# Optimization experiments

Measured on AMD Instinct MI355X. Metric: run time of the kernel, lower is better.

## Reference

```python
import jax, jax.numpy as jnp
import numpy as np

MARGIN = 0.2
LAMBDA_CLS = 1.0
LAMBDA_TRIPLET = 1.0
EPS = 1e-6  # matches torch pairwise_distance eps inside TripletMarginLoss
B, D, C = 8192, 192, 1024


def setup_inputs() -> dict:
    key = jax.random.key(0)
    k1, k2, k3 = jax.random.split(key, 3)
    embeddings = jax.random.normal(k1, (B, D), dtype=jnp.float32)
    logits = jax.random.normal(k2, (B, C), dtype=jnp.float32)
    targets = jax.random.randint(k3, (B,), 0, C, dtype=jnp.int64)
    return {"embeddings": embeddings, "logits": logits, "targets": targets}


def reference(embeddings, logits, targets):
    # ---- classification loss: mean cross entropy ----
    logp = jax.nn.log_softmax(logits, axis=-1)
    cls_loss = -jnp.mean(jnp.take_along_axis(logp, targets[:, None], axis=1))

    # ---- vectorized hard triplet mining (mining='hard'), on detached embeddings ----
    e = jax.lax.stop_gradient(embeddings)
    sq = jnp.sum(e * e, axis=1)                       # [B]
    d2 = sq[:, None] + sq[None, :] - 2.0 * (e @ e.T)  # [B, B]
    dist = jnp.sqrt(jnp.maximum(d2, 0.0))

    same = targets[:, None] == targets[None, :]       # [B, B]
    eye = jnp.eye(targets.shape[0], dtype=bool)
    pos_mask = same & ~eye
    neg_mask = ~same
    valid = pos_mask.any(axis=1) & neg_mask.any(axis=1)

    # hard positive: farthest same-speaker; hard negative: closest other-speaker
    pos_idx = jnp.argmax(jnp.where(pos_mask, dist, -jnp.inf), axis=1)
    neg_idx = jnp.argmin(jnp.where(neg_mask, dist, jnp.inf), axis=1)

    # ---- triplet margin loss on live embeddings ----
    a = embeddings
    p = embeddings[pos_idx]
    n = embeddings[neg_idx]
    d_ap = jnp.linalg.norm(a - p + EPS, axis=1)
    d_an = jnp.linalg.norm(a - n + EPS, axis=1)
    per_triplet = jnp.maximum(d_ap - d_an + MARGIN, 0.0)

    w = valid.astype(per_triplet.dtype)
    cnt = jnp.sum(w)
    trip_loss = jnp.where(cnt > 0, jnp.sum(per_triplet * w) / jnp.maximum(cnt, 1.0), 0.0)

    return LAMBDA_CLS * cls_loss + LAMBDA_TRIPLET * trip_loss
```

## Files before the change

kernel.cpp:

```cpp
#include <hip/hip_runtime.h>
#include <math.h>

#define B_N    8192
#define D_DIM  192
#define C_CLS  1024
#define MARGIN 0.2f
#define EPS_T  1e-6f

#define TI     64
#define TJ     128
#define JSPLIT 16
#define JLEN   (B_N / JSPLIT)
#define RB     384

typedef short v8s  __attribute__((ext_vector_type(8)));
typedef float v16f __attribute__((ext_vector_type(16)));

typedef __attribute__((address_space(3))) unsigned int       lds_u32;
typedef __attribute__((address_space(1))) const unsigned int glb_u32;

__device__ __forceinline__ void gll16(const void* g, void* l) {
  __builtin_amdgcn_global_load_lds((glb_u32*)g, (lds_u32*)l, 16, 0, 0);
}

__device__ __forceinline__ int swzb(int r, int cb) {
  return r * RB + (cb ^ ((r & 7) << 4));
}

__device__ __forceinline__ unsigned fkey(float f) {
  unsigned u = __float_as_uint(f);
  return (u & 0x80000000u) ? ~u : (u | 0x80000000u);
}

__device__ __forceinline__ unsigned short to_bf(float x) {
  unsigned u = __float_as_uint(x);
  u += 0x7fffu + ((u >> 16) & 1u);
  return (unsigned short)(u >> 16);
}

__global__ __launch_bounds__(256) void prep_kernel(
    const float* __restrict__ e, unsigned short* __restrict__ ebf,
    float* __restrict__ sq,
    unsigned long long* __restrict__ posw, unsigned long long* __restrict__ negw,
    float* __restrict__ accum) {
  int w = threadIdx.x >> 6, lane = threadIdx.x & 63;
  int row = blockIdx.x * 4 + w;
  const float* p = e + (size_t)row * D_DIM;
  float v0 = p[lane], v1 = p[lane + 64], v2 = p[lane + 128];
  unsigned short* q = ebf + (size_t)row * D_DIM;
  q[lane] = to_bf(v0); q[lane + 64] = to_bf(v1); q[lane + 128] = to_bf(v2);
  float s = v0 * v0 + v1 * v1 + v2 * v2;
  #pragma unroll
  for (int off = 32; off; off >>= 1) s += __shfl_xor(s, off);
  if (lane == 0) sq[row] = s;
  int b = blockIdx.x;
  if (b < 32)       posw[b * 256 + threadIdx.x] = 0ULL;
  else if (b < 64)  negw[(b - 32) * 256 + threadIdx.x] = ~0ULL;
  else if (b == 64 && threadIdx.x < 4) ((unsigned*)accum)[threadIdx.x] = 0u;
}

__global__ __launch_bounds__(256, 2) void mine_kernel(
    const unsigned short* __restrict__ ebf, const int* __restrict__ tgt,
    const float* __restrict__ sq, const float* __restrict__ logits,
    unsigned long long* __restrict__ posw, unsigned long long* __restrict__ negw,
    float* __restrict__ accum) {
  __shared__ unsigned short lds_b[TJ * (RB / 2)];
  __shared__ int   lds_t[TJ];
  __shared__ float lds_s[TJ];
  __shared__ unsigned long long pmrg[TI];
  __shared__ unsigned long long nmrg[TI];
  __shared__ float ce_part[4];

  const int tid  = threadIdx.x;
  const int w    = tid >> 6;
  const int lane = tid & 63;
  const int n5   = lane & 31;
  const int h    = lane >> 5;
  const int i0 = blockIdx.x * TI;
  const int jb = blockIdx.y * JLEN;

  char* ldsc = (char*)lds_b;

  if (tid < TI) { pmrg[tid] = 0ULL; nmrg[tid] = ~0ULL; }

  {
    const char* src = (const char*)(ebf + (size_t)i0 * D_DIM);
    #pragma unroll
    for (int t = 0; t < 6; ++t) {
      int c  = t * 256 + tid;
      int r  = c / 24;
      int cb = (c - r * 24) * 16;
      gll16(src + r * RB + (cb ^ ((r & 7) << 4)),
            ldsc + (t * 256 + (tid & ~63)) * 16);
    }
  }
  __syncthreads();
  v8s bfrag[2][12];
  #pragma unroll
  for (int tb = 0; tb < 2; ++tb)
    #pragma unroll
    for (int kc = 0; kc < 12; ++kc)
      bfrag[tb][kc] = *(const v8s*)(ldsc + swzb(tb * 32 + n5, kc * 32 + h * 16));

  int my_t[2];
  #pragma unroll
  for (int tb = 0; tb < 2; ++tb) my_t[tb] = tgt[i0 + tb * 32 + n5];

  float    pv[2] = {-3.4e38f, -3.4e38f}, nv[2] = {3.4e38f, 3.4e38f};
  unsigned pi_[2] = {0u, 0u}, ni_[2] = {0xFFFFFFFFu, 0xFFFFFFFFu};

  for (int j0 = jb; j0 < jb + JLEN; j0 += TJ) {
    __syncthreads();
    {
      const char* src = (const char*)(ebf + (size_t)j0 * D_DIM);
      #pragma unroll
      for (int t = 0; t < 12; ++t) {
        int c  = t * 256 + tid;
        int r  = c / 24;
        int cb = (c - r * 24) * 16;
        gll16(src + r * RB + (cb ^ ((r & 7) << 4)),
              ldsc + (t * 256 + (tid & ~63)) * 16);
      }
    }
    if (tid < TJ) { lds_t[tid] = tgt[j0 + tid]; lds_s[tid] = sq[j0 + tid]; }
    __syncthreads();

    v16f acc[2];
    #pragma unroll
    for (int tb = 0; tb < 2; ++tb)
      #pragma unroll
      for (int r = 0; r < 16; ++r) acc[tb][r] = 0.f;

    #pragma unroll
    for (int kc = 0; kc < 12; ++kc) {
      v8s afr = *(const v8s*)(ldsc + swzb(w * 32 + n5, kc * 32 + h * 16));
      acc[0] = __builtin_amdgcn_mfma_f32_32x32x16_bf16(afr, bfrag[0][kc], acc[0], 0, 0, 0);
      acc[1] = __builtin_amdgcn_mfma_f32_32x32x16_bf16(afr, bfrag[1][kc], acc[1], 0, 0, 0);
    }

    #pragma unroll
    for (int p = 0; p < 4; ++p) {
      int jb4 = w * 32 + p * 8 + h * 4;
      float4 s4 = *(const float4*)&lds_s[jb4];
      int4   t4 = *(const int4*)&lds_t[jb4];
      #pragma unroll
      for (int q = 0; q < 4; ++q) {
        float sv = (q == 0) ? s4.x : (q == 1) ? s4.y : (q == 2) ? s4.z : s4.w;
        int   tv = (q == 0) ? t4.x : (q == 1) ? t4.y : (q == 2) ? t4.z : t4.w;
        unsigned jg = (unsigned)(j0 + jb4 + q);
        #pragma unroll
        for (int tb = 0; tb < 2; ++tb) {
          float val = fmaf(acc[tb][p * 4 + q], -2.0f, sv);
          bool same = (tv == my_t[tb]);
          float vp = same ? val : -3.4e38f;
          float vn = same ? 3.4e38f : val;
          if (vp > pv[tb]) { pv[tb] = vp; pi_[tb] = jg; }
          if (vn < nv[tb]) { nv[tb] = vn; ni_[tb] = jg; }
        }
      }
    }
  }

  #pragma unroll
  for (int tb = 0; tb < 2; ++tb) {
    unsigned long long pk =
        ((unsigned long long)fkey(pv[tb]) << 32) | (unsigned long long)(unsigned)(~pi_[tb]);
    unsigned long long nk =
        ((unsigned long long)fkey(nv[tb]) << 32) | (unsigned long long)ni_[tb];
    unsigned long long po = __shfl_xor(pk, 32);
    unsigned long long no = __shfl_xor(nk, 32);
    pk = pk > po ? pk : po;
    nk = nk < no ? nk : no;
    if (h == 0) {
      atomicMax(&pmrg[tb * 32 + n5], pk);
      atomicMin(&nmrg[tb * 32 + n5], nk);
    }
  }
  __syncthreads();
  if (tid < TI) {
    atomicMax(&posw[i0 + tid], pmrg[tid]);
    atomicMin(&negw[i0 + tid], nmrg[tid]);
  }

  {
    int row = (blockIdx.y * 128 + blockIdx.x) * 4 + w;
    const float* lp = logits + (size_t)row * C_CLS;
    float4 x[4];
    #pragma unroll
    for (int t = 0; t < 4; ++t) x[t] = *(const float4*)(lp + lane * 4 + 256 * t);
    float m = -3.4e38f;
    #pragma unroll
    for (int t = 0; t < 4; ++t)
      m = fmaxf(m, fmaxf(fmaxf(x[t].x, x[t].y), fmaxf(x[t].z, x[t].w)));
    #pragma unroll
    for (int off = 32; off; off >>= 1) m = fmaxf(m, __shfl_xor(m, off));
    float s = 0.f;
    #pragma unroll
    for (int t = 0; t < 4; ++t)
      s += __expf(x[t].x - m) + __expf(x[t].y - m) +
           __expf(x[t].z - m) + __expf(x[t].w - m);
    #pragma unroll
    for (int off = 32; off; off >>= 1) s += __shfl_xor(s, off);
    if (lane == 0) ce_part[w] = m + __logf(s) - lp[tgt[row]];
  }
  __syncthreads();
  if (tid == 0)
    atomicAdd(&accum[0], ce_part[0] + ce_part[1] + ce_part[2] + ce_part[3]);
}

__global__ __launch_bounds__(1024) void trip_fin_kernel(
    const float* __restrict__ e,
    const unsigned long long* __restrict__ posw,
    const unsigned long long* __restrict__ negw,
    float* __restrict__ accum, float* __restrict__ out) {
  __shared__ float ssum[16];
  __shared__ float scnt[16];
  int w = threadIdx.x >> 6, lane = threadIdx.x & 63;
  int i = blockIdx.x * 16 + w;
  unsigned long long pp = posw[i], np = negw[i];
  unsigned pidx = ~(unsigned)pp;
  unsigned nidx = (unsigned)np;
  float res = 0.f, c = 0.f;
  if (pp != 0ULL && np != ~0ULL && pidx != (unsigned)i) {
    const float* pa = e + (size_t)i * D_DIM;
    const float* pb = e + (size_t)pidx * D_DIM;
    const float* pc = e + (size_t)nidx * D_DIM;
    float dap = 0.f, dan = 0.f;
    #pragma unroll
    for (int t = 0; t < 3; ++t) {
      int k = lane + 64 * t;
      float av = pa[k];
      float d1 = av - pb[k] + EPS_T;
      float d2 = av - pc[k] + EPS_T;
      dap += d1 * d1;
      dan += d2 * d2;
    }
    #pragma unroll
    for (int off = 32; off; off >>= 1) {
      dap += __shfl_xor(dap, off);
      dan += __shfl_xor(dan, off);
    }
    res = fmaxf(sqrtf(dap) - sqrtf(dan) + MARGIN, 0.f);
    c = 1.f;
  }
  if (lane == 0) { ssum[w] = res; scnt[w] = c; }
  __syncthreads();
  if (threadIdx.x == 0) {
    float a = 0.f, b = 0.f;
    #pragma unroll
    for (int k = 0; k < 16; ++k) { a += ssum[k]; b += scnt[k]; }
    atomicAdd(&accum[1], a);
    atomicAdd(&accum[2], b);
    __threadfence();
    unsigned old = atomicAdd((unsigned*)&accum[3], 1u);
    if (old == 511u) {
      __threadfence();
      float cls = atomicAdd(&accum[0], 0.f);
      float ts  = atomicAdd(&accum[1], 0.f);
      float tc  = atomicAdd(&accum[2], 0.f);
      float trip = (tc > 0.f) ? ts / fmaxf(tc, 1.f) : 0.f;
      out[0] = cls / (float)B_N + trip;
    }
  }
}

extern "C" void kernel_launch(void* const* d_in, const int* in_sizes, int n_in,
                              void* d_out, int out_size, void* d_ws, size_t ws_size,
                              hipStream_t stream) {
  const float* emb    = (const float*)d_in[0];
  const float* logits = (const float*)d_in[1];
  const int*   tgt    = (const int*)d_in[2];
  float* out = (float*)d_out;

  char* ws = (char*)d_ws;
  unsigned short* ebf = (unsigned short*)ws;
  unsigned long long* posw = (unsigned long long*)(ws + 3145728);
  unsigned long long* negw = (unsigned long long*)(ws + 3145728 + 65536);
  float* sq    = (float*)(ws + 3145728 + 131072);
  float* accum = (float*)(ws + 3145728 + 163840);

  prep_kernel<<<2048, 256, 0, stream>>>(emb, ebf, sq, posw, negw, accum);
  mine_kernel<<<dim3(B_N / TI, JSPLIT), 256, 0, stream>>>(ebf, tgt, sq, logits, posw, negw, accum);
  trip_fin_kernel<<<512, 1024, 0, stream>>>(emb, posw, negw, accum, out);
}
```

Before: 159.3 us.

## Double-buffer j-tiles in LDS and enlarge the i-tile to 512-thread blocks

The mining kernel now uses 512-thread blocks covering 128 anchor rows and 4 j-splits, down from 64 rows and 16 splits. This halves how often each j-tile is re-read from memory across blocks. J-tiles, targets and norms are double-buffered in LDS, so the async load of the next tile overlaps the MFMA and argmax work on the current one, with one barrier per iteration. The cross-entropy part is redistributed so each wave handles four logit rows. The cost is more LDS per block and one block per CU, which leaves less room for inter-block latency hiding.

```diff
diff --git a/kernel.cpp b/kernel.cpp
--- a/kernel.cpp
+++ b/kernel.cpp
@@ -7,10 +7,11 @@
 #define MARGIN 0.2f
 #define EPS_T  1e-6f
 
-#define TI     64
+#define TI     128
 #define TJ     128
-#define JSPLIT 16
+#define JSPLIT 4
 #define JLEN   (B_N / JSPLIT)
+#define NT     (JLEN / TJ)
 #define RB     384
 
 typedef short v8s  __attribute__((ext_vector_type(8)));
@@ -25,6 +26,17 @@
 
 __device__ __forceinline__ int swzb(int r, int cb) {
   return r * RB + (cb ^ ((r & 7) << 4));
+}
+
+__device__ __forceinline__ void stage_tile(char* dst, const char* src, int tid) {
+  #pragma unroll
+  for (int k = 0; k < 6; ++k) {
+    int c  = k * 512 + tid;
+    int r  = c / 24;
+    int cb = (c - r * 24) * 16;
+    gll16(src + r * RB + (cb ^ ((r & 7) << 4)),
+          dst + (k * 512 + (tid & ~63)) * 16);
+  }
 }
 
 __device__ __forceinline__ unsigned fkey(float f) {
@@ -59,71 +71,63 @@
   else if (b == 64 && threadIdx.x < 4) ((unsigned*)accum)[threadIdx.x] = 0u;
 }
 
-__global__ __launch_bounds__(256, 2) void mine_kernel(
+__global__ __launch_bounds__(512, 1) void mine_kernel(
     const unsigned short* __restrict__ ebf, const int* __restrict__ tgt,
     const float* __restrict__ sq, const float* __restrict__ logits,
     unsigned long long* __restrict__ posw, unsigned long long* __restrict__ negw,
     float* __restrict__ accum) {
-  __shared__ unsigned short lds_b[TJ * (RB / 2)];
-  __shared__ int   lds_t[TJ];
-  __shared__ float lds_s[TJ];
+  __shared__ unsigned short buf[2][TJ * (RB / 2)];
+  __shared__ int   lds_t[2][TJ];
+  __shared__ float lds_s[2][TJ];
   __shared__ unsigned long long pmrg[TI];
   __shared__ unsigned long long nmrg[TI];
-  __shared__ float ce_part[4];
+  __shared__ float ce_part[8];
 
   const int tid  = threadIdx.x;
   const int w    = tid >> 6;
   const int lane = tid & 63;
   const int n5   = lane & 31;
   const int h    = lane >> 5;
+  const int wj   = w & 3;
+  const int wi   = w >> 2;
   const int i0 = blockIdx.x * TI;
   const int jb = blockIdx.y * JLEN;
 
-  char* ldsc = (char*)lds_b;
+  char* bufA = (char*)buf[0];
+  char* bufB = (char*)buf[1];
 
   if (tid < TI) { pmrg[tid] = 0ULL; nmrg[tid] = ~0ULL; }
 
-  {
-    const char* src = (const char*)(ebf + (size_t)i0 * D_DIM);
-    #pragma unroll
-    for (int t = 0; t < 6; ++t) {
-      int c  = t * 256 + tid;
-      int r  = c / 24;
-      int cb = (c - r * 24) * 16;
-      gll16(src + r * RB + (cb ^ ((r & 7) << 4)),
-            ldsc + (t * 256 + (tid & ~63)) * 16);
-    }
-  }
-  __syncthreads();
+  stage_tile(bufB, (const char*)(ebf + (size_t)i0 * D_DIM), tid);
+  stage_tile(bufA, (const char*)(ebf + (size_t)jb * D_DIM), tid);
+  if (tid < TJ) { lds_t[0][tid] = tgt[jb + tid]; lds_s[0][tid] = sq[jb + tid]; }
+  __syncthreads();
+
   v8s bfrag[2][12];
   #pragma unroll
   for (int tb = 0; tb < 2; ++tb)
     #pragma unroll
     for (int kc = 0; kc < 12; ++kc)
-      bfrag[tb][kc] = *(const v8s*)(ldsc + swzb(tb * 32 + n5, kc * 32 + h * 16));
+      bfrag[tb][kc] = *(const v8s*)(bufB + swzb(wi * 64 + tb * 32 + n5, kc * 32 + h * 16));
 
   int my_t[2];
   #pragma unroll
-  for (int tb = 0; tb < 2; ++tb) my_t[tb] = tgt[i0 + tb * 32 + n5];
+  for (int tb = 0; tb < 2; ++tb) my_t[tb] = tgt[i0 + wi * 64 + tb * 32 + n5];
+
+  __syncthreads();
 
   float    pv[2] = {-3.4e38f, -3.4e38f}, nv[2] = {3.4e38f, 3.4e38f};
   unsigned pi_[2] = {0u, 0u}, ni_[2] = {0xFFFFFFFFu, 0xFFFFFFFFu};
 
-  for (int j0 = jb; j0 < jb + JLEN; j0 += TJ) {
-    __syncthreads();
-    {
-      const char* src = (const char*)(ebf + (size_t)j0 * D_DIM);
-      #pragma unroll
-      for (int t = 0; t < 12; ++t) {
-        int c  = t * 256 + tid;
-        int r  = c / 24;
-        int cb = (c - r * 24) * 16;
-        gll16(src + r * RB + (cb ^ ((r & 7) << 4)),
-              ldsc + (t * 256 + (tid & ~63)) * 16);
-      }
-    }
-    if (tid < TJ) { lds_t[tid] = tgt[j0 + tid]; lds_s[tid] = sq[j0 + tid]; }
-    __syncthreads();
+  for (int t = 0; t < NT; ++t) {
+    const int cur = t & 1;
+    char* cbuf = (char*)buf[cur];
+
+    if (t + 1 < NT) {
+      int jn = jb + (t + 1) * TJ;
+      stage_tile((char*)buf[cur ^ 1], (const char*)(ebf + (size_t)jn * D_DIM), tid);
+      if (tid < TJ) { lds_t[cur ^ 1][tid] = tgt[jn + tid]; lds_s[cur ^ 1][tid] = sq[jn + tid]; }
+    }
 
     v16f acc[2];
     #pragma unroll
@@ -133,16 +137,17 @@
 
     #pragma unroll
     for (int kc = 0; kc < 12; ++kc) {
-      v8s afr = *(const v8s*)(ldsc + swzb(w * 32 + n5, kc * 32 + h * 16));
+      v8s afr = *(const v8s*)(cbuf + swzb(wj * 32 + n5, kc * 32 + h * 16));
       acc[0] = __builtin_amdgcn_mfma_f32_32x32x16_bf16(afr, bfrag[0][kc], acc[0], 0, 0, 0);
       acc[1] = __builtin_amdgcn_mfma_f32_32x32x16_bf16(afr, bfrag[1][kc], acc[1], 0, 0, 0);
     }
 
+    const int j0 = jb + t * TJ;
     #pragma unroll
     for (int p = 0; p < 4; ++p) {
-      int jb4 = w * 32 + p * 8 + h * 4;
-      float4 s4 = *(const float4*)&lds_s[jb4];
-      int4   t4 = *(const int4*)&lds_t[jb4];
+      int jb4 = wj * 32 + p * 8 + h * 4;
+      float4 s4 = *(const float4*)&lds_s[cur][jb4];
+      int4   t4 = *(const int4*)&lds_t[cur][jb4];
       #pragma unroll
       for (int q = 0; q < 4; ++q) {
         float sv = (q == 0) ? s4.x : (q == 1) ? s4.y : (q == 2) ? s4.z : s4.w;
@@ -159,6 +164,8 @@
         }
       }
     }
+
+    __syncthreads();
   }
 
   #pragma unroll
@@ -172,8 +179,8 @@
     pk = pk > po ? pk : po;
     nk = nk < no ? nk : no;
     if (h == 0) {
-      atomicMax(&pmrg[tb * 32 + n5], pk);
-      atomicMin(&nmrg[tb * 32 + n5], nk);
+      atomicMax(&pmrg[wi * 64 + tb * 32 + n5], pk);
+      atomicMin(&nmrg[wi * 64 + tb * 32 + n5], nk);
     }
   }
   __syncthreads();
@@ -183,29 +190,39 @@
   }
 
   {
-    int row = (blockIdx.y * 128 + blockIdx.x) * 4 + w;
-    const float* lp = logits + (size_t)row * C_CLS;
-    float4 x[4];
-    #pragma unroll
-    for (int t = 0; t < 4; ++t) x[t] = *(const float4*)(lp + lane * 4 + 256 * t);
-    float m = -3.4e38f;
-    #pragma unroll
-    for (int t = 0; t < 4; ++t)
-      m = fmaxf(m, fmaxf(fmaxf(x[t].x, x[t].y), fmaxf(x[t].z, x[t].w)));
-    #pragma unroll
-    for (int off = 32; off; off >>= 1) m = fmaxf(m, __shfl_xor(m, off));
-    float s = 0.f;
-    #pragma unroll
-    for (int t = 0; t < 4; ++t)
-      s += __expf(x[t].x - m) + __expf(x[t].y - m) +
-           __expf(x[t].z - m) + __expf(x[t].w - m);
-    #pragma unroll
-    for (int off = 32; off; off >>= 1) s += __shfl_xor(s, off);
-    if (lane == 0) ce_part[w] = m + __logf(s) - lp[tgt[row]];
-  }
-  __syncthreads();
-  if (tid == 0)
-    atomicAdd(&accum[0], ce_part[0] + ce_part[1] + ce_part[2] + ce_part[3]);
+    int blin = blockIdx.y * 64 + blockIdx.x;
+    float ce_acc = 0.f;
+    #pragma unroll
+    for (int it = 0; it < 4; ++it) {
+      int row = blin * 32 + w * 4 + it;
+      const float* lp = logits + (size_t)row * C_CLS;
+      float4 x[4];
+      #pragma unroll
+      for (int u = 0; u < 4; ++u) x[u] = *(const float4*)(lp + lane * 4 + 256 * u);
+      float m = -3.4e38f;
+      #pragma unroll
+      for (int u = 0; u < 4; ++u)
+        m = fmaxf(m, fmaxf(fmaxf(x[u].x, x[u].y), fmaxf(x[u].z, x[u].w)));
+      #pragma unroll
+      for (int off = 32; off; off >>= 1) m = fmaxf(m, __shfl_xor(m, off));
+      float s = 0.f;
+      #pragma unroll
+      for (int u = 0; u < 4; ++u)
+        s += __expf(x[u].x - m) + __expf(x[u].y - m) +
+             __expf(x[u].z - m) + __expf(x[u].w - m);
+      #pragma unroll
+      for (int off = 32; off; off >>= 1) s += __shfl_xor(s, off);
+      if (lane == 0) ce_acc += m + __logf(s) - lp[tgt[row]];
+    }
+    if (lane == 0) ce_part[w] = ce_acc;
+  }
+  __syncthreads();
+  if (tid == 0) {
+    float a = 0.f;
+    #pragma unroll
+    for (int k = 0; k < 8; ++k) a += ce_part[k];
+    atomicAdd(&accum[0], a);
+  }
 }
 
 __global__ __launch_bounds__(1024) void trip_fin_kernel(
@@ -280,6 +297,6 @@
   float* accum = (float*)(ws + 3145728 + 163840);
 
   prep_kernel<<<2048, 256, 0, stream>>>(emb, ebf, sq, posw, negw, accum);
-  mine_kernel<<<dim3(B_N / TI, JSPLIT), 256, 0, stream>>>(ebf, tgt, sq, logits, posw, negw, accum);
+  mine_kernel<<<dim3(B_N / TI, JSPLIT), 512, 0, stream>>>(ebf, tgt, sq, logits, posw, negw, accum);
   trip_fin_kernel<<<512, 1024, 0, stream>>>(emb, posw, negw, accum, out);
 }
```

After: 150.7 us. 1.06x faster.
